# Performance work log

Measured on AMD Instinct MI355X. Metric: run time of the kernel, lower is better.

The kernel has to match this reference:

```python
import jax, jax.numpy as jnp
import numpy as np

N_EMBED = 1024
N_HEADS = 16
HEAD_DIM = N_EMBED // N_HEADS


def setup_inputs() -> dict:
    key = jax.random.key(0)
    ks = jax.random.split(key, 5)
    B, T, C = 4, 2048, N_EMBED
    s_in = 1.0 / np.sqrt(C)
    x = jax.random.normal(ks[0], (B, T, C), dtype=jnp.float32)
    W_qkv = jax.random.normal(ks[1], (C, 3 * C), dtype=jnp.float32) * s_in
    b_qkv = jnp.zeros((3 * C,), dtype=jnp.float32)
    W_out = jax.random.normal(ks[2], (C, C), dtype=jnp.float32) * s_in
    b_out = jnp.zeros((C,), dtype=jnp.float32)
    return {"x": x, "W_qkv": W_qkv, "b_qkv": b_qkv, "W_out": W_out, "b_out": b_out}


def reference(x, W_qkv, b_qkv, W_out, b_out):
    B, T, C = x.shape
    H, D = N_HEADS, HEAD_DIM
    qkv = x @ W_qkv + b_qkv                       # [B,T,3C]
    q, k, v = jnp.split(qkv, 3, axis=-1)
    # [B,T,C] -> [B,H,T,D]
    q = q.reshape(B, T, H, D).transpose(0, 2, 1, 3)
    k = k.reshape(B, T, H, D).transpose(0, 2, 1, 3)
    v = v.reshape(B, T, H, D).transpose(0, 2, 1, 3)
    scale = 1.0 / np.sqrt(D)
    attn = jnp.einsum('bhqd,bhkd->bhqk', q, k) * scale   # [B,H,T,T]
    causal = jnp.tril(jnp.ones((T, T), dtype=bool))
    attn = jnp.where(causal, attn, -jnp.inf)
    attn = jax.nn.softmax(attn, axis=-1)
    out = jnp.einsum('bhqk,bhkd->bhqd', attn, v)          # [B,H,T,D]
    out = out.transpose(0, 2, 1, 3).reshape(B, T, C)
    return out @ W_out + b_out
```

## Files before the change

kernel.cpp:

```cpp
#include <hip/hip_runtime.h>
#include <stdint.h>

#define BB 4
#define TT 2048
#define CC 1024
#define HH 16
#define DD 64
#define MM (BB*TT)

typedef __bf16 bf16x8 __attribute__((ext_vector_type(8)));
typedef float  f32x4  __attribute__((ext_vector_type(4)));

__device__ __forceinline__ unsigned short f2bf(float f) {
  __bf16 h = (__bf16)f;
  union { __bf16 h; unsigned short u; } c; c.h = h;
  return c.u;
}

__device__ __forceinline__ void glds16(const void* g, void* l) {
  __builtin_amdgcn_global_load_lds((const __attribute__((address_space(1))) void*)g,
                                   (__attribute__((address_space(3))) void*)l,
                                   16, 0, 0);
}

__device__ __forceinline__ void perm32swap(uint32_t& a, uint32_t& b) {
  asm volatile("v_permlane32_swap_b32 %0, %1" : "+v"(a), "+v"(b));
}
__device__ __forceinline__ void perm16swap(uint32_t& a, uint32_t& b) {
  asm volatile("v_permlane16_swap_b32 %0, %1" : "+v"(a), "+v"(b));
}

__device__ __forceinline__ int xcd_swz(int bid, int nwg) {
  if (nwg & 7) return bid;
  return (bid & 7) * (nwg >> 3) + (bid >> 3);
}

typedef unsigned short u16x8 __attribute__((ext_vector_type(8)));
__global__ void f32_to_bf16_kn(const float* __restrict__ in,
                               unsigned short* __restrict__ out, int n) {
  int i = (blockIdx.x * blockDim.x + threadIdx.x) * 8;
  const int stride = gridDim.x * blockDim.x * 8;
  for (; i < n; i += stride) {
    float4 a = *(const float4*)&in[i];
    float4 b = *(const float4*)&in[i + 4];
    u16x8 t;
    t[0]=f2bf(a.x); t[1]=f2bf(a.y); t[2]=f2bf(a.z); t[3]=f2bf(a.w);
    t[4]=f2bf(b.x); t[5]=f2bf(b.y); t[6]=f2bf(b.z); t[7]=f2bf(b.w);
    *(u16x8*)&out[i] = t;
  }
}

__global__ void transpose_to_bf16(const float* __restrict__ in,
                                  unsigned short* __restrict__ out,
                                  int R, int Cc) {
  __shared__ float tile[32][33];
  const int c0 = blockIdx.x * 32, r0 = blockIdx.y * 32;
  const int tx = threadIdx.x & 31, ty = threadIdx.x >> 5;
#pragma unroll
  for (int i = 0; i < 32; i += 8)
    tile[ty + i][tx] = in[(size_t)(r0 + ty + i) * Cc + c0 + tx];
  __syncthreads();
#pragma unroll
  for (int i = 0; i < 32; i += 8)
    out[(size_t)(c0 + ty + i) * R + r0 + tx] = f2bf(tile[tx][ty + i]);
}

template<int MODE>
__global__ void gemm128(const unsigned short* __restrict__ A,
                        const unsigned short* __restrict__ Bt,
                        const float* __restrict__ bias,
                        void* __restrict__ outp,
                        int M, int N, int K)
{
  __shared__ unsigned short Alds[2][128 * 32];
  __shared__ unsigned short Blds[2][128 * 32];
  const int tid = threadIdx.x;
  const int lane = tid & 63;
  const int wid  = tid >> 6;
  const int wm = wid >> 1, wn = wid & 1;
  const int nwg = (int)(gridDim.x * gridDim.y);
  const int swz = xcd_swz((int)(blockIdx.y * gridDim.x + blockIdx.x), nwg);
  const int m0 = (swz / (int)gridDim.x) * 128;
  const int n0 = (swz % (int)gridDim.x) * 128;
  const int l15 = lane & 15, l4 = lane >> 4;

  const size_t soffA = (size_t)(m0 + l15) * K + l4 * 8;
  const size_t soffB = (size_t)(n0 + l15) * K + l4 * 8;

  f32x4 acc[4][4];
#pragma unroll
  for (int i = 0; i < 4; i++)
#pragma unroll
    for (int j = 0; j < 4; j++) acc[i][j] = (f32x4){0.f, 0.f, 0.f, 0.f};

#pragma unroll
  for (int c2 = 0; c2 < 2; c2++) {
    const int c = wid * 2 + c2;
    glds16(A  + soffA + (size_t)c * 16 * K, (char*)&Alds[0][0] + c * 1024);
    glds16(Bt + soffB + (size_t)c * 16 * K, (char*)&Blds[0][0] + c * 1024);
  }

  const int NT = K >> 5;
  for (int t = 0; t < NT; t++) {
    __syncthreads();
    if (t + 1 < NT) {
      const int nb = (t + 1) & 1;
      const int k1 = (t + 1) * 32;
#pragma unroll
      for (int c2 = 0; c2 < 2; c2++) {
        const int c = wid * 2 + c2;
        glds16(A  + soffA + (size_t)c * 16 * K + k1, (char*)&Alds[nb][0] + c * 1024);
        glds16(Bt + soffB + (size_t)c * 16 * K + k1, (char*)&Blds[nb][0] + c * 1024);
      }
    }
    const int cb = t & 1;
    bf16x8 af[4], bfr[4];
#pragma unroll
    for (int i = 0; i < 4; i++)
      af[i]  = *(const bf16x8*)&Alds[cb][(wm * 4 + i) * 512 + lane * 8];
#pragma unroll
    for (int j = 0; j < 4; j++)
      bfr[j] = *(const bf16x8*)&Blds[cb][(wn * 4 + j) * 512 + lane * 8];
    __builtin_amdgcn_s_setprio(1);
#pragma unroll
    for (int i = 0; i < 4; i++)
#pragma unroll
      for (int j = 0; j < 4; j++)
        acc[i][j] = __builtin_amdgcn_mfma_f32_16x16x32_bf16(af[i], bfr[j], acc[i][j], 0, 0, 0);
    __builtin_amdgcn_s_setprio(0);
  }

#pragma unroll
  for (int i = 0; i < 4; i++) {
#pragma unroll
    for (int j = 0; j < 4; j++) {
      const int n = n0 + wn * 64 + j * 16 + l15;
      const float bn = bias[n];
#pragma unroll
      for (int r = 0; r < 4; r++) {
        const int m = m0 + wm * 64 + i * 16 + l4 * 4 + r;
        float v = acc[i][j][r] + bn;
        if (MODE == 0) {
          unsigned short* qb = (unsigned short*)outp;
          const int which = n >> 10;
          const int cc = n & 1023;
          const int h = cc >> 6, d = cc & 63;
          const int b = m >> 11, t = m & 2047;
          if (which == 0) {
            const size_t off = (((size_t)(b * HH + h)) * TT + t) * DD + d;
            qb[off] = f2bf(v * 0.125f);
          } else if (which == 1) {
            const size_t off = (((size_t)(b * HH + h)) * TT + t) * DD + d;
            qb[(size_t)MM * CC + off] = f2bf(v);
          } else {
            const size_t offv = (((size_t)(b * HH + h)) * DD + d) * TT + t;
            qb[(size_t)2 * MM * CC + offv] = f2bf(v);
          }
        } else {
          float* O = (float*)outp;
          O[(size_t)m * N + n] = v;
        }
      }
    }
  }
}

__global__ void attn_fwd(const unsigned short* __restrict__ qbuf,
                         const unsigned short* __restrict__ kbuf,
                         const unsigned short* __restrict__ vtbuf,
                         unsigned short* __restrict__ ao)
{
  __shared__ unsigned short Klds[2][64 * 64];
  __shared__ unsigned short Vt[2][64 * 64];
  const int tid = threadIdx.x, lane = tid & 63, w = tid >> 6;
  const int l15 = lane & 15, l4 = lane >> 4;
  const int NQT = TT / 64;
  const int nwg = NQT * BB * HH;
  const int swz = xcd_swz((int)blockIdx.x, nwg);
  const int bh = swz / NQT;
  const int qtile = NQT - 1 - (swz % NQT);
  const int q0 = qtile * 64;
  const unsigned short* Qb  = qbuf  + (size_t)bh * TT * DD;
  const unsigned short* Kb  = kbuf  + (size_t)bh * TT * DD;
  const unsigned short* VTb = vtbuf + (size_t)bh * DD * TT;

  const int srow = lane >> 3;
  const int scol = ((lane & 7) ^ srow) * 8;

  bf16x8 qf[2];
#pragma unroll
  for (int ks = 0; ks < 2; ks++)
    qf[ks] = *(const bf16x8*)&Qb[(size_t)(q0 + w * 16 + l15) * DD + ks * 32 + l4 * 8];

  f32x4 o[4];
#pragma unroll
  for (int df = 0; df < 4; df++) o[df] = (f32x4){0.f, 0.f, 0.f, 0.f};
  float m_st = -__builtin_huge_valf();
  float l_st = 0.f;

  const int qwmin = q0 + w * 16;
  const int qrow  = qwmin + l15;
  const int nt = qtile + 1;

#pragma unroll
  for (int j = 0; j < 2; j++) {
    const int g = w * 2 + j;
    const int row = g * 8 + srow;
    glds16(Kb + (size_t)row * DD + scol,       (char*)&Klds[0][0] + g * 1024);
    glds16(VTb + (size_t)row * TT + scol,      (char*)&Vt[0][0]   + g * 1024);
  }

  for (int t = 0; t < nt; t++) {
    __syncthreads();
    if (t + 1 < nt) {
      const int kv1 = (t + 1) * 64;
      const int nb = (t + 1) & 1;
#pragma unroll
      for (int j = 0; j < 2; j++) {
        const int g = w * 2 + j;
        const int row = g * 8 + srow;
        glds16(Kb + (size_t)(kv1 + row) * DD + scol, (char*)&Klds[nb][0] + g * 1024);
        glds16(VTb + (size_t)row * TT + kv1 + scol,  (char*)&Vt[nb][0]   + g * 1024);
      }
    }
    const int cb = t & 1;
    const int kv0 = t * 64;

    if (kv0 <= qwmin + 15) {
      f32x4 s[4];
      __builtin_amdgcn_s_setprio(1);
#pragma unroll
      for (int fc = 0; fc < 4; fc++) {
        s[fc] = (f32x4){0.f, 0.f, 0.f, 0.f};
        const int kr = fc * 16 + l15;
#pragma unroll
        for (int ks = 0; ks < 2; ks++) {
          bf16x8 kf = *(const bf16x8*)&Klds[cb][(kr * 64 + ks * 32 + l4 * 8) ^ ((kr & 7) << 3)];
          s[fc] = __builtin_amdgcn_mfma_f32_16x16x32_bf16(kf, qf[ks], s[fc], 0, 0, 0);
        }
      }
      __builtin_amdgcn_s_setprio(0);
      if (kv0 + 63 > qwmin) {
#pragma unroll
        for (int fc = 0; fc < 4; fc++)
#pragma unroll
          for (int r = 0; r < 4; r++)
            if (kv0 + fc * 16 + l4 * 4 + r > qrow) s[fc][r] = -__builtin_huge_valf();
      }
      float tm = s[0][0];
#pragma unroll
      for (int fc = 0; fc < 4; fc++)
#pragma unroll
        for (int r = 0; r < 4; r++) tm = fmaxf(tm, s[fc][r]);
      tm = fmaxf(tm, __shfl_xor(tm, 16));
      tm = fmaxf(tm, __shfl_xor(tm, 32));
      const float mn = fmaxf(m_st, tm);
      const float sc = __expf(m_st - mn);
      m_st = mn;
      float rs = 0.f;
      uint32_t wpk[4][2];
#pragma unroll
      for (int fc = 0; fc < 4; fc++) {
        float p0 = __expf(s[fc][0] - mn), p1 = __expf(s[fc][1] - mn);
        float p2 = __expf(s[fc][2] - mn), p3 = __expf(s[fc][3] - mn);
        rs += (p0 + p1) + (p2 + p3);
        union { unsigned short u[2]; uint32_t d; } a, b;
        a.u[0] = f2bf(p0); a.u[1] = f2bf(p1);
        b.u[0] = f2bf(p2); b.u[1] = f2bf(p3);
        wpk[fc][0] = a.d; wpk[fc][1] = b.d;
      }
      rs += __shfl_xor(rs, 16);
      rs += __shfl_xor(rs, 32);
      l_st = l_st * sc + rs;
#pragma unroll
      for (int df = 0; df < 4; df++)
#pragma unroll
        for (int r = 0; r < 4; r++) o[df][r] *= sc;
      bf16x8 pa[2];
#pragma unroll
      for (int ks = 0; ks < 2; ks++) {
        uint32_t Aq = wpk[2 * ks][0], Bq = wpk[2 * ks][1];
        uint32_t Cq = wpk[2 * ks + 1][0], Dq = wpk[2 * ks + 1][1];
        perm32swap(Aq, Cq); perm16swap(Aq, Cq);
        perm32swap(Bq, Dq); perm16swap(Bq, Dq);
        union { uint32_t d[4]; bf16x8 v; } pf;
        pf.d[0] = Aq; pf.d[1] = Bq; pf.d[2] = Cq; pf.d[3] = Dq;
        pa[ks] = pf.v;
      }
      __builtin_amdgcn_s_setprio(1);
#pragma unroll
      for (int df = 0; df < 4; df++) {
        const int d = df * 16 + l15;
#pragma unroll
        for (int ks = 0; ks < 2; ks++) {
          bf16x8 vf = *(const bf16x8*)&Vt[cb][(d * 64 + ks * 32 + l4 * 8) ^ ((d & 7) << 3)];
          o[df] = __builtin_amdgcn_mfma_f32_16x16x32_bf16(vf, pa[ks], o[df], 0, 0, 0);
        }
      }
      __builtin_amdgcn_s_setprio(0);
    }
  }

  const int b = bh >> 4, h = bh & 15;
  const float inv = 1.0f / l_st;
#pragma unroll
  for (int df = 0; df < 4; df++)
#pragma unroll
    for (int r = 0; r < 4; r++) {
      const int d = df * 16 + l4 * 4 + r;
      ao[((size_t)(b * TT + qrow)) * CC + h * DD + d] = f2bf(o[df][r] * inv);
    }
}

extern "C" void kernel_launch(void* const* d_in, const int* in_sizes, int n_in,
                              void* d_out, int out_size, void* d_ws, size_t ws_size,
                              hipStream_t stream) {
  const float* x    = (const float*)d_in[0];
  const float* Wqkv = (const float*)d_in[1];
  const float* bqkv = (const float*)d_in[2];
  const float* Wout = (const float*)d_in[3];
  const float* bout = (const float*)d_in[4];
  float* out = (float*)d_out;
  char* ws = (char*)d_ws;

  unsigned short* xb    = (unsigned short*)ws;
  unsigned short* wqkvt = (unsigned short*)(ws + 16777216);
  unsigned short* woutt = (unsigned short*)(ws + 23068672);
  unsigned short* qkv   = (unsigned short*)(ws + 25165824);
  unsigned short* ao    = xb;

  f32_to_bf16_kn<<<2048, 256, 0, stream>>>(x, xb, MM * CC);
  transpose_to_bf16<<<dim3(3 * CC / 32, CC / 32), 256, 0, stream>>>(Wqkv, wqkvt, CC, 3 * CC);
  transpose_to_bf16<<<dim3(CC / 32, CC / 32), 256, 0, stream>>>(Wout, woutt, CC, CC);

  gemm128<0><<<dim3(3 * CC / 128, MM / 128), 256, 0, stream>>>(
      xb, wqkvt, bqkv, (void*)qkv, MM, 3 * CC, CC);

  attn_fwd<<<(TT / 64) * BB * HH, 256, 0, stream>>>(
      qkv, qkv + (size_t)MM * CC, qkv + (size_t)2 * MM * CC, ao);

  gemm128<1><<<dim3(CC / 128, MM / 128), 256, 0, stream>>>(
      ao, woutt, bout, (void*)out, MM, CC, CC);
}
```

Before: 342.7 us.

## Replace double-buffered K=32 GEMM loop with single-buffered K=64 tiles

The GEMM main loop drops the double-buffered 32-wide K prefetch in favour of a single 64-wide K tile. Each iteration loads the tile, waits on a barrier, then issues 32 MFMAs. This halves the number of loop iterations and barrier pairs per tile of work, but global loads no longer overlap with compute. The setprio hints are removed as well.

```diff
diff --git a/kernel.cpp b/kernel.cpp
--- a/kernel.cpp
+++ b/kernel.cpp
@@ -72,8 +72,8 @@
                         void* __restrict__ outp,
                         int M, int N, int K)
 {
-  __shared__ unsigned short Alds[2][128 * 32];
-  __shared__ unsigned short Blds[2][128 * 32];
+  __shared__ unsigned short Alds[128 * 64];
+  __shared__ unsigned short Blds[128 * 64];
   const int tid = threadIdx.x;
   const int lane = tid & 63;
   const int wid  = tid >> 6;
@@ -93,41 +93,35 @@
 #pragma unroll
     for (int j = 0; j < 4; j++) acc[i][j] = (f32x4){0.f, 0.f, 0.f, 0.f};
 
-#pragma unroll
-  for (int c2 = 0; c2 < 2; c2++) {
-    const int c = wid * 2 + c2;
-    glds16(A  + soffA + (size_t)c * 16 * K, (char*)&Alds[0][0] + c * 1024);
-    glds16(Bt + soffB + (size_t)c * 16 * K, (char*)&Blds[0][0] + c * 1024);
-  }
-
-  const int NT = K >> 5;
-  for (int t = 0; t < NT; t++) {
+  for (int k0 = 0; k0 < K; k0 += 64) {
     __syncthreads();
-    if (t + 1 < NT) {
-      const int nb = (t + 1) & 1;
-      const int k1 = (t + 1) * 32;
-#pragma unroll
-      for (int c2 = 0; c2 < 2; c2++) {
-        const int c = wid * 2 + c2;
-        glds16(A  + soffA + (size_t)c * 16 * K + k1, (char*)&Alds[nb][0] + c * 1024);
-        glds16(Bt + soffB + (size_t)c * 16 * K + k1, (char*)&Blds[nb][0] + c * 1024);
-      }
-    }
-    const int cb = t & 1;
-    bf16x8 af[4], bfr[4];
+#pragma unroll
+    for (int c2 = 0; c2 < 2; c2++) {
+      const int rb = wid * 2 + c2;
+#pragma unroll
+      for (int ks = 0; ks < 2; ks++) {
+        glds16(A  + soffA + (size_t)rb * 16 * K + k0 + ks * 32,
+               (char*)Alds + (rb * 2 + ks) * 1024);
+        glds16(Bt + soffB + (size_t)rb * 16 * K + k0 + ks * 32,
+               (char*)Blds + (rb * 2 + ks) * 1024);
+      }
+    }
+    __syncthreads();
+    bf16x8 af[4][2], bfr[4][2];
 #pragma unroll
     for (int i = 0; i < 4; i++)
-      af[i]  = *(const bf16x8*)&Alds[cb][(wm * 4 + i) * 512 + lane * 8];
-#pragma unroll
-    for (int j = 0; j < 4; j++)
-      bfr[j] = *(const bf16x8*)&Blds[cb][(wn * 4 + j) * 512 + lane * 8];
-    __builtin_amdgcn_s_setprio(1);
-#pragma unroll
-    for (int i = 0; i < 4; i++)
-#pragma unroll
-      for (int j = 0; j < 4; j++)
-        acc[i][j] = __builtin_amdgcn_mfma_f32_16x16x32_bf16(af[i], bfr[j], acc[i][j], 0, 0, 0);
-    __builtin_amdgcn_s_setprio(0);
+#pragma unroll
+      for (int ks = 0; ks < 2; ks++) {
+        af[i][ks]  = *(const bf16x8*)&Alds[((wm * 4 + i) * 2 + ks) * 512 + lane * 8];
+        bfr[i][ks] = *(const bf16x8*)&Blds[((wn * 4 + i) * 2 + ks) * 512 + lane * 8];
+      }
+#pragma unroll
+    for (int ks = 0; ks < 2; ks++)
+#pragma unroll
+      for (int i = 0; i < 4; i++)
+#pragma unroll
+        for (int j = 0; j < 4; j++)
+          acc[i][j] = __builtin_amdgcn_mfma_f32_16x16x32_bf16(af[i][ks], bfr[j][ks], acc[i][j], 0, 0, 0);
   }
 
 #pragma unroll
```

After: 336.5 us. Within noise of the previous version (-1.8%).
